# Performance work log

Hardware: AMD Instinct MI355X
Metric: run time of the kernel (lower is better)

Reference implementation:

```python
import jax, jax.numpy as jnp
import numpy as np
import math

B, N = 1, 512
C_S, C_Z = 384, 128
H, D, PQ, PV = 12, 16, 4, 8
W_C = math.sqrt(2.0 / (9.0 * PQ))
W_L = math.sqrt(1.0 / 3.0)
OUT_IN = H * D + H * PV * 3 + H * PV + H * C_Z  # 2112


def setup_inputs() -> dict:
    key = jax.random.key(0)
    ks = jax.random.split(key, 16)
    s = 0.02
    return {
        "single_representation": jax.random.normal(ks[0], (B, N, C_S), jnp.float32),
        "pair_representation": jax.random.normal(ks[1], (B, N, N, C_Z), jnp.float32),
        "rotations": jax.random.normal(ks[2], (B, N, 3, 3), jnp.float32),
        "translation": jax.random.normal(ks[3], (B, N, 3), jnp.float32),
        "w_q": jax.random.normal(ks[4], (C_S, H * D), jnp.float32) * s,
        "w_k": jax.random.normal(ks[5], (C_S, H * D), jnp.float32) * s,
        "w_v": jax.random.normal(ks[6], (C_S, H * D), jnp.float32) * s,
        "w_qf": jax.random.normal(ks[7], (C_S, 3 * H * PQ), jnp.float32) * s,
        "w_kf": jax.random.normal(ks[8], (C_S, 3 * H * PQ), jnp.float32) * s,
        "w_vf": jax.random.normal(ks[9], (C_S, 3 * H * PV), jnp.float32) * s,
        "w_bias": jax.random.normal(ks[10], (C_Z, H), jnp.float32) * s,
        "head_weights": jnp.zeros((H,), jnp.float32),
        "w_out": jax.random.normal(ks[11], (OUT_IN, C_S), jnp.float32) * s,
        "b_out": jnp.zeros((C_S,), jnp.float32),
    }


def reference(single_representation, pair_representation, rotations, translation,
              w_q, w_k, w_v, w_qf, w_kf, w_vf, w_bias, head_weights, w_out, b_out):
    s = single_representation
    z = pair_representation
    b, n, _ = s.shape

    # scalar q/k/v  [b, n, H, D]
    Q = (s @ w_q).reshape(b, n, H, D)
    K = (s @ w_k).reshape(b, n, H, D)
    V = (s @ w_v).reshape(b, n, H, D)

    # point q/k/v in local frames  [b, n, H, P, 3]
    Qf = (s @ w_qf).reshape(b, n, H, PQ, 3)
    Kf = (s @ w_kf).reshape(b, n, H, PQ, 3)
    Vf = (s @ w_vf).reshape(b, n, H, PV, 3)

    bias = z @ w_bias  # [b, n, n, H]

    # lift points to the global frame
    gq = jnp.einsum('biop,bihqp->bihqo', rotations, Qf) + translation[:, :, None, None, :]
    gk = jnp.einsum('biop,bihqp->bihqo', rotations, Kf) + translation[:, :, None, None, :]

    diff = gq[:, :, None] - gk[:, None]            # [b, i, j, H, PQ, 3]
    gamma = jax.nn.softplus(head_weights)          # [H]
    point_scores = (-0.5 * W_C) * gamma[None, None, None, :] * jnp.sum(diff * diff, axis=(-1, -2))

    rep_scores = jnp.einsum('bihd,bjhd->bijh', Q, K) / math.sqrt(D) + bias
    scores = W_L * (rep_scores + point_scores)     # [b, i, j, H]
    attn = jax.nn.softmax(scores, axis=-2)         # softmax over j

    out_pair = jnp.einsum('bijh,bijd->bihd', attn, z)          # [b, n, H, C_Z]
    out_rep = jnp.einsum('bijh,bjhd->bhid', attn, V)           # [b, H, n, D]

    gv = jnp.einsum('biop,bihqp->bihqo', rotations, Vf) + translation[:, :, None, None, :]
    tmp = jnp.einsum('bijh,bjhqo->bhiqo', attn, gv)            # [b, H, n, PV, 3]

    R_inv = jnp.swapaxes(rotations, -1, -2)
    t_inv = -jnp.einsum('bira,bia->bir', R_inv, translation)
    out_vals = jnp.einsum('biop,bhiqp->bhiqo', R_inv, tmp) + t_inv[:, None, :, None, :]

    out_rep = jnp.transpose(out_rep, (0, 2, 1, 3)).reshape(b, n, H * D)
    out_vals = jnp.transpose(out_vals, (0, 2, 1, 3, 4)).reshape(b, n, H * PV * 3)
    out_norms = jnp.sqrt(jnp.sum(out_vals.reshape(b, n, H * PV, 3) ** 2, axis=-1) + 1e-8)
    out_pair = out_pair.reshape(b, n, H * C_Z)

    cat = jnp.concatenate([out_rep, out_vals, out_norms, out_pair], axis=-1)
    return cat @ w_out + b_out
```

## Files before the change

### kernel.cpp

```cpp
#include <hip/hip_runtime.h>
#include <math.h>

#define N    512
#define CS   384
#define CZ   128
#define H    12
#define D    16
#define PQ   4
#define PV   8
#define CAT_W 2112

#define WC 0.23570226039551584f
#define WL 0.5773502691896258f

#define O_Q    0
#define O_KT   98304
#define O_VT   196608
#define O_QF   294912
#define O_KF   368640
#define O_VF   442368
#define O_GQ   589824
#define O_GKT  663552
#define O_GVT  737280
#define O_BIAS 884736
#define O_PART O_BIAS
#define O_CAT  4030464

#define KSPLIT 8
#define KCH    264
#define ALD    516

__global__ __launch_bounds__(256) void k_proj(
    const float* __restrict__ s,
    const float* __restrict__ wq, const float* __restrict__ wk,
    const float* __restrict__ wv, const float* __restrict__ wqf,
    const float* __restrict__ wkf, const float* __restrict__ wvf,
    float* __restrict__ ws) {
  int id = blockIdx.x * 256 + threadIdx.x;
  int i = id / 1152, p = id % 1152;
  const float* w; int col, W; float* dst;
  if (p < 192)      { w = wq;  col = p;     W = 192; dst = ws + O_Q  + i*192 + col; }
  else if (p < 384) { w = wk;  col = p-192; W = 192; dst = ws + O_KT + col*512 + i; }
  else if (p < 576) { w = wv;  col = p-384; W = 192; dst = ws + O_VT + col*512 + i; }
  else if (p < 720) { w = wqf; col = p-576; W = 144; dst = ws + O_QF + i*144 + col; }
  else if (p < 864) { w = wkf; col = p-720; W = 144; dst = ws + O_KF + i*144 + col; }
  else              { w = wvf; col = p-864; W = 288; dst = ws + O_VF + i*288 + col; }
  const float* srow = s + i*CS;
  float acc = 0.f;
  #pragma unroll 8
  for (int k = 0; k < CS; ++k) acc += srow[k] * w[k*W + col];
  *dst = acc;
}

__global__ __launch_bounds__(256) void k_lift(
    const float* __restrict__ rot, const float* __restrict__ trans,
    float* __restrict__ ws) {
  int id = blockIdx.x * 256 + threadIdx.x;
  int i = id / 192, pt = id % 192;
  const float* R = rot + i*9;
  const float* T = trans + i*3;
  if (pt < 48) {
    const float* src = ws + O_QF + i*144 + pt*3;
    float l0 = src[0], l1 = src[1], l2 = src[2];
    float* dst = ws + O_GQ + i*144 + pt*3;
    #pragma unroll
    for (int o = 0; o < 3; ++o)
      dst[o] = R[o*3+0]*l0 + R[o*3+1]*l1 + R[o*3+2]*l2 + T[o];
  } else if (pt < 96) {
    int p3 = pt - 48;
    const float* src = ws + O_KF + i*144 + p3*3;
    float l0 = src[0], l1 = src[1], l2 = src[2];
    #pragma unroll
    for (int o = 0; o < 3; ++o)
      ws[O_GKT + (p3*3+o)*512 + i] = R[o*3+0]*l0 + R[o*3+1]*l1 + R[o*3+2]*l2 + T[o];
  } else {
    int p3 = pt - 96;
    const float* src = ws + O_VF + i*288 + p3*3;
    float l0 = src[0], l1 = src[1], l2 = src[2];
    #pragma unroll
    for (int o = 0; o < 3; ++o)
      ws[O_GVT + (p3*3+o)*512 + i] = R[o*3+0]*l0 + R[o*3+1]*l1 + R[o*3+2]*l2 + T[o];
  }
}

__global__ __launch_bounds__(256) void k_bias(
    const float* __restrict__ z, const float* __restrict__ wb,
    float* __restrict__ ws) {
  __shared__ float wbl[CZ*H];
  int t = threadIdx.x;
  for (int idx = t; idx < CZ*H; idx += 256) wbl[idx] = wb[idx];
  __syncthreads();
  int row = blockIdx.x * 64 + (t >> 2);
  int q = t & 3;
  const float4* zr = (const float4*)(z + (size_t)row * CZ) + q;
  float acc[H];
  #pragma unroll
  for (int h = 0; h < H; ++h) acc[h] = 0.f;
  #pragma unroll
  for (int kk = 0; kk < 8; ++kk) {
    float4 v = zr[kk*4];
    int c = (q + kk*4) * 4;
    #pragma unroll
    for (int h = 0; h < H; ++h)
      acc[h] += v.x*wbl[(c+0)*H+h] + v.y*wbl[(c+1)*H+h]
              + v.z*wbl[(c+2)*H+h] + v.w*wbl[(c+3)*H+h];
  }
  #pragma unroll
  for (int h = 0; h < H; ++h) {
    acc[h] += __shfl_xor(acc[h], 1);
    acc[h] += __shfl_xor(acc[h], 2);
  }
  if (q == 0) {
    int i = row >> 9, j = row & 511;
    float* bT = ws + O_BIAS + (size_t)i*6144 + j;
    #pragma unroll
    for (int h = 0; h < H; ++h) bT[(size_t)h*512] = acc[h];
  }
}

__global__ __launch_bounds__(256) void k_score(
    const float* __restrict__ hw, float* __restrict__ ws) {
  __shared__ float Qi[192];
  __shared__ float gqi[144];
  __shared__ float coef[H];
  int i = blockIdx.x;
  int t = threadIdx.x;
  int wave = t >> 6, lane = t & 63;
  if (t < 192) Qi[t]  = ws[O_Q  + (size_t)i*192 + t];
  if (t < 144) gqi[t] = ws[O_GQ + (size_t)i*144 + t];
  if (t < H) {
    float x = hw[t];
    float sp = fmaxf(x, 0.f) + log1pf(__expf(-fabsf(x)));
    coef[t] = -0.5f * WC * sp;
  }
  __syncthreads();
  float* att = ws + O_BIAS + (size_t)i*6144;
  const float* Kt  = ws + O_KT;
  const float* gkT = ws + O_GKT;
  for (int hh = 0; hh < 3; ++hh) {
    int h = wave*3 + hh;
    float sreg[8];
    float cf = coef[h];
    #pragma unroll
    for (int jb = 0; jb < 8; ++jb) {
      int j = jb*64 + lane;
      float rep = 0.f;
      #pragma unroll
      for (int d = 0; d < 16; ++d) rep += Qi[h*16+d] * Kt[(h*16+d)*512 + j];
      float pt = 0.f;
      #pragma unroll
      for (int r = 0; r < 12; ++r) {
        float df = gqi[h*12+r] - gkT[(h*12+r)*512 + j];
        pt += df*df;
      }
      sreg[jb] = WL * (rep * 0.25f + att[(size_t)h*512 + j] + cf*pt);
    }
    float m = sreg[0];
    #pragma unroll
    for (int jb = 1; jb < 8; ++jb) m = fmaxf(m, sreg[jb]);
    #pragma unroll
    for (int off = 32; off; off >>= 1) m = fmaxf(m, __shfl_xor(m, off));
    float e = 0.f;
    #pragma unroll
    for (int jb = 0; jb < 8; ++jb) { sreg[jb] = __expf(sreg[jb] - m); e += sreg[jb]; }
    #pragma unroll
    for (int off = 32; off; off >>= 1) e += __shfl_xor(e, off);
    float inv = 1.f / e;
    #pragma unroll
    for (int jb = 0; jb < 8; ++jb) att[(size_t)h*512 + jb*64 + lane] = sreg[jb] * inv;
  }
}

__global__ __launch_bounds__(256) void k_apply(
    const float* __restrict__ z, const float* __restrict__ rot,
    const float* __restrict__ trans, float* __restrict__ ws) {
  __shared__ float aL[H*ALD];
  __shared__ float pairOdd[H*128];
  __shared__ float tmpP[H*PV*3];
  int i = blockIdx.x;
  int t = threadIdx.x;
  const float* attn = ws + O_BIAS + (size_t)i*6144;
  for (int idx = t; idx < 6144; idx += 256)
    aL[(idx >> 9)*ALD + (idx & 511)] = attn[idx];
  __syncthreads();
  float* cat = ws + O_CAT + (size_t)i*CAT_W;

  for (int task = t; task < 480; task += 256) {
    int u, h; const float* src;
    if (task < 192) { u = task;       h = u >> 4; src = ws + O_VT  + (size_t)u*512; }
    else            { u = task - 192; h = u / 24; src = ws + O_GVT + (size_t)u*512; }
    const float4* a4 = (const float4*)(aL + h*ALD);
    const float4* s4 = (const float4*)src;
    float4 acc4 = {0.f, 0.f, 0.f, 0.f};
    #pragma unroll 8
    for (int j4 = 0; j4 < 128; ++j4) {
      float4 a = a4[j4], v = s4[j4];
      acc4.x += a.x*v.x; acc4.y += a.y*v.y; acc4.z += a.z*v.z; acc4.w += a.w*v.w;
    }
    float acc = (acc4.x + acc4.y) + (acc4.z + acc4.w);
    if (task < 192) cat[u] = acc; else tmpP[u] = acc;
  }

  {
    int c = t & 127, g = t >> 7;
    float acc[H];
    #pragma unroll
    for (int h = 0; h < H; ++h) acc[h] = 0.f;
    const float* zr = z + (size_t)i*N*CZ + c;
    #pragma unroll 4
    for (int jj = 0; jj < 256; ++jj) {
      int j = jj*2 + g;
      float zv = zr[(size_t)j*CZ];
      #pragma unroll
      for (int h = 0; h < H; ++h) acc[h] += aL[h*ALD + j] * zv;
    }
    if (g) {
      #pragma unroll
      for (int h = 0; h < H; ++h) pairOdd[h*128 + c] = acc[h];
    }
    __syncthreads();
    if (!g) {
      #pragma unroll
      for (int h = 0; h < H; ++h) cat[576 + h*128 + c] = acc[h] + pairOdd[h*128 + c];
    }
  }

  if (t < 96) {
    int h = t >> 3, q = t & 7;
    const float* R = rot + i*9;
    float tp[3];
    #pragma unroll
    for (int p = 0; p < 3; ++p) tp[p] = tmpP[h*24 + q*3 + p] - trans[i*3 + p];
    float nrm = 1e-8f;
    #pragma unroll
    for (int o = 0; o < 3; ++o) {
      float v = R[o]*tp[0] + R[3+o]*tp[1] + R[6+o]*tp[2];
      cat[192 + h*24 + q*3 + o] = v;
      nrm += v*v;
    }
    cat[480 + h*8 + q] = sqrtf(nrm);
  }
}

__global__ __launch_bounds__(128) void k_out_part(
    const float* __restrict__ wo, const float* __restrict__ ws,
    float* __restrict__ part) {
  __shared__ float catT[KCH][16];
  int rt = blockIdx.x, ct = blockIdx.y, kc = blockIdx.z;
  int t = threadIdx.x;
  int i0 = rt * 16;
  int c  = ct * 128 + t;
  int k0 = kc * KCH;
  const float* cat = ws + O_CAT;
  for (int idx = t; idx < 16*KCH; idx += 128) {
    int r = idx / KCH, k = idx % KCH;
    catT[k][r] = cat[(size_t)(i0 + r) * CAT_W + k0 + k];
  }
  __syncthreads();
  float acc[16];
  #pragma unroll
  for (int r = 0; r < 16; ++r) acc[r] = 0.f;
  const float* wp = wo + (size_t)k0 * 384 + c;
  #pragma unroll 4
  for (int k = 0; k < KCH; ++k) {
    float wv = wp[(size_t)k * 384];
    const float* a = catT[k];
    #pragma unroll
    for (int r = 0; r < 16; ++r) acc[r] += a[r] * wv;
  }
  float* dst = part + (size_t)kc * (N*CS) + (size_t)i0 * 384 + c;
  #pragma unroll
  for (int r = 0; r < 16; ++r) dst[(size_t)r * 384] = acc[r];
}

__global__ __launch_bounds__(256) void k_out_red(
    const float* __restrict__ bo, const float* __restrict__ ws,
    float* __restrict__ out) {
  int id = blockIdx.x * 256 + threadIdx.x;
  int c4 = id % 96;
  float4 acc = ((const float4*)bo)[c4];
  const float* part = ws + O_PART;
  #pragma unroll
  for (int s = 0; s < KSPLIT; ++s) {
    float4 p = *(const float4*)(part + (size_t)s * (N*CS) + (size_t)id * 4);
    acc.x += p.x; acc.y += p.y; acc.z += p.z; acc.w += p.w;
  }
  ((float4*)out)[id] = acc;
}

extern "C" void kernel_launch(void* const* d_in, const int* in_sizes, int n_in,
                              void* d_out, int out_size, void* d_ws, size_t ws_size,
                              hipStream_t stream) {
  const float* s     = (const float*)d_in[0];
  const float* z     = (const float*)d_in[1];
  const float* rot   = (const float*)d_in[2];
  const float* trans = (const float*)d_in[3];
  const float* wq    = (const float*)d_in[4];
  const float* wk    = (const float*)d_in[5];
  const float* wv    = (const float*)d_in[6];
  const float* wqf   = (const float*)d_in[7];
  const float* wkf   = (const float*)d_in[8];
  const float* wvf   = (const float*)d_in[9];
  const float* wb    = (const float*)d_in[10];
  const float* hw    = (const float*)d_in[11];
  const float* wo    = (const float*)d_in[12];
  const float* bo    = (const float*)d_in[13];
  float* out = (float*)d_out;
  float* ws  = (float*)d_ws;

  hipLaunchKernelGGL(k_proj, dim3(512*1152/256), dim3(256), 0, stream,
                     s, wq, wk, wv, wqf, wkf, wvf, ws);
  hipLaunchKernelGGL(k_lift, dim3(512*192/256), dim3(256), 0, stream,
                     rot, trans, ws);
  hipLaunchKernelGGL(k_bias, dim3(512*512/64), dim3(256), 0, stream,
                     z, wb, ws);
  hipLaunchKernelGGL(k_score, dim3(512), dim3(256), 0, stream,
                     hw, ws);
  hipLaunchKernelGGL(k_apply, dim3(512), dim3(256), 0, stream,
                     z, rot, trans, ws);
  hipLaunchKernelGGL(k_out_part, dim3(32, 3, KSPLIT), dim3(128), 0, stream,
                     wo, ws, ws + O_PART);
  hipLaunchKernelGGL(k_out_red, dim3(192), dim3(256), 0, stream,
                     bo, ws, out);
}
```

Before: 497.6 us.

## Widen score/apply blocks to 768 threads and register-tile projection GEMV

The projection kernel now computes four output columns for two rows per thread using float4 weight loads, which raises reuse of the weight loads. The score kernel uses 768 threads, one wave per head, instead of looping over three heads per wave. The apply kernel uses 768 threads: 512 handle the V and point-value reductions split across 8 lanes with shuffle reductions, and 256 handle the pair-representation reduction using float4 z loads and shuffles. The shared-memory attention row padding changes from 516 to 520. Larger blocks may reduce occupancy, and the float4 pair accumulators add register pressure.

```diff
diff --git a/kernel.cpp b/kernel.cpp
--- a/kernel.cpp
+++ b/kernel.cpp
@@ -28,7 +28,7 @@
 
 #define KSPLIT 8
 #define KCH    264
-#define ALD    516
+#define ALD    520
 
 __global__ __launch_bounds__(256) void k_proj(
     const float* __restrict__ s,
@@ -37,19 +37,50 @@
     const float* __restrict__ wkf, const float* __restrict__ wvf,
     float* __restrict__ ws) {
   int id = blockIdx.x * 256 + threadIdx.x;
-  int i = id / 1152, p = id % 1152;
-  const float* w; int col, W; float* dst;
-  if (p < 192)      { w = wq;  col = p;     W = 192; dst = ws + O_Q  + i*192 + col; }
-  else if (p < 384) { w = wk;  col = p-192; W = 192; dst = ws + O_KT + col*512 + i; }
-  else if (p < 576) { w = wv;  col = p-384; W = 192; dst = ws + O_VT + col*512 + i; }
-  else if (p < 720) { w = wqf; col = p-576; W = 144; dst = ws + O_QF + i*144 + col; }
-  else if (p < 864) { w = wkf; col = p-720; W = 144; dst = ws + O_KF + i*144 + col; }
-  else              { w = wvf; col = p-864; W = 288; dst = ws + O_VF + i*288 + col; }
-  const float* srow = s + i*CS;
-  float acc = 0.f;
+  int i0 = id / 288;
+  int c4 = id % 288;
+  int col = c4 * 4;
+  const float* w; int cc, W, kind;
+  if (col < 192)      { w = wq;  cc = col;     W = 192; kind = 0; }
+  else if (col < 384) { w = wk;  cc = col-192; W = 192; kind = 1; }
+  else if (col < 576) { w = wv;  cc = col-384; W = 192; kind = 2; }
+  else if (col < 720) { w = wqf; cc = col-576; W = 144; kind = 3; }
+  else if (col < 864) { w = wkf; cc = col-720; W = 144; kind = 4; }
+  else                { w = wvf; cc = col-864; W = 288; kind = 5; }
+  const float* s0 = s + (size_t)i0 * CS;
+  const float* s1 = s0 + 256 * CS;
+  float4 a0 = {0,0,0,0}, a1 = {0,0,0,0};
   #pragma unroll 8
-  for (int k = 0; k < CS; ++k) acc += srow[k] * w[k*W + col];
-  *dst = acc;
+  for (int k = 0; k < CS; ++k) {
+    float4 wv4 = *(const float4*)(w + (size_t)k * W + cc);
+    float x0 = s0[k], x1 = s1[k];
+    a0.x += x0*wv4.x; a0.y += x0*wv4.y; a0.z += x0*wv4.z; a0.w += x0*wv4.w;
+    a1.x += x1*wv4.x; a1.y += x1*wv4.y; a1.z += x1*wv4.z; a1.w += x1*wv4.w;
+  }
+  int i1 = i0 + 256;
+  if (kind == 0) {
+    *(float4*)(ws + O_Q + (size_t)i0*192 + cc) = a0;
+    *(float4*)(ws + O_Q + (size_t)i1*192 + cc) = a1;
+  } else if (kind == 1) {
+    ws[O_KT + (size_t)(cc+0)*512 + i0] = a0.x; ws[O_KT + (size_t)(cc+1)*512 + i0] = a0.y;
+    ws[O_KT + (size_t)(cc+2)*512 + i0] = a0.z; ws[O_KT + (size_t)(cc+3)*512 + i0] = a0.w;
+    ws[O_KT + (size_t)(cc+0)*512 + i1] = a1.x; ws[O_KT + (size_t)(cc+1)*512 + i1] = a1.y;
+    ws[O_KT + (size_t)(cc+2)*512 + i1] = a1.z; ws[O_KT + (size_t)(cc+3)*512 + i1] = a1.w;
+  } else if (kind == 2) {
+    ws[O_VT + (size_t)(cc+0)*512 + i0] = a0.x; ws[O_VT + (size_t)(cc+1)*512 + i0] = a0.y;
+    ws[O_VT + (size_t)(cc+2)*512 + i0] = a0.z; ws[O_VT + (size_t)(cc+3)*512 + i0] = a0.w;
+    ws[O_VT + (size_t)(cc+0)*512 + i1] = a1.x; ws[O_VT + (size_t)(cc+1)*512 + i1] = a1.y;
+    ws[O_VT + (size_t)(cc+2)*512 + i1] = a1.z; ws[O_VT + (size_t)(cc+3)*512 + i1] = a1.w;
+  } else if (kind == 3) {
+    *(float4*)(ws + O_QF + (size_t)i0*144 + cc) = a0;
+    *(float4*)(ws + O_QF + (size_t)i1*144 + cc) = a1;
+  } else if (kind == 4) {
+    *(float4*)(ws + O_KF + (size_t)i0*144 + cc) = a0;
+    *(float4*)(ws + O_KF + (size_t)i1*144 + cc) = a1;
+  } else {
+    *(float4*)(ws + O_VF + (size_t)i0*288 + cc) = a0;
+    *(float4*)(ws + O_VF + (size_t)i1*288 + cc) = a1;
+  }
 }
 
 __global__ __launch_bounds__(256) void k_lift(
@@ -72,14 +103,14 @@
     float l0 = src[0], l1 = src[1], l2 = src[2];
     #pragma unroll
     for (int o = 0; o < 3; ++o)
-      ws[O_GKT + (p3*3+o)*512 + i] = R[o*3+0]*l0 + R[o*3+1]*l1 + R[o*3+2]*l2 + T[o];
+      ws[O_GKT + (size_t)(p3*3+o)*512 + i] = R[o*3+0]*l0 + R[o*3+1]*l1 + R[o*3+2]*l2 + T[o];
   } else {
     int p3 = pt - 96;
     const float* src = ws + O_VF + i*288 + p3*3;
     float l0 = src[0], l1 = src[1], l2 = src[2];
     #pragma unroll
     for (int o = 0; o < 3; ++o)
-      ws[O_GVT + (p3*3+o)*512 + i] = R[o*3+0]*l0 + R[o*3+1]*l1 + R[o*3+2]*l2 + T[o];
+      ws[O_GVT + (size_t)(p3*3+o)*512 + i] = R[o*3+0]*l0 + R[o*3+1]*l1 + R[o*3+2]*l2 + T[o];
   }
 }
 
@@ -118,112 +149,126 @@
   }
 }
 
-__global__ __launch_bounds__(256) void k_score(
+__global__ __launch_bounds__(768) void k_score(
     const float* __restrict__ hw, float* __restrict__ ws) {
   __shared__ float Qi[192];
   __shared__ float gqi[144];
-  __shared__ float coef[H];
   int i = blockIdx.x;
   int t = threadIdx.x;
-  int wave = t >> 6, lane = t & 63;
+  int h = t >> 6, lane = t & 63;
   if (t < 192) Qi[t]  = ws[O_Q  + (size_t)i*192 + t];
-  if (t < 144) gqi[t] = ws[O_GQ + (size_t)i*144 + t];
-  if (t < H) {
-    float x = hw[t];
-    float sp = fmaxf(x, 0.f) + log1pf(__expf(-fabsf(x)));
-    coef[t] = -0.5f * WC * sp;
-  }
-  __syncthreads();
-  float* att = ws + O_BIAS + (size_t)i*6144;
-  const float* Kt  = ws + O_KT;
-  const float* gkT = ws + O_GKT;
-  for (int hh = 0; hh < 3; ++hh) {
-    int h = wave*3 + hh;
-    float sreg[8];
-    float cf = coef[h];
-    #pragma unroll
-    for (int jb = 0; jb < 8; ++jb) {
-      int j = jb*64 + lane;
-      float rep = 0.f;
-      #pragma unroll
-      for (int d = 0; d < 16; ++d) rep += Qi[h*16+d] * Kt[(h*16+d)*512 + j];
-      float pt = 0.f;
-      #pragma unroll
-      for (int r = 0; r < 12; ++r) {
-        float df = gqi[h*12+r] - gkT[(h*12+r)*512 + j];
-        pt += df*df;
-      }
-      sreg[jb] = WL * (rep * 0.25f + att[(size_t)h*512 + j] + cf*pt);
-    }
-    float m = sreg[0];
-    #pragma unroll
-    for (int jb = 1; jb < 8; ++jb) m = fmaxf(m, sreg[jb]);
-    #pragma unroll
-    for (int off = 32; off; off >>= 1) m = fmaxf(m, __shfl_xor(m, off));
-    float e = 0.f;
-    #pragma unroll
-    for (int jb = 0; jb < 8; ++jb) { sreg[jb] = __expf(sreg[jb] - m); e += sreg[jb]; }
-    #pragma unroll
-    for (int off = 32; off; off >>= 1) e += __shfl_xor(e, off);
-    float inv = 1.f / e;
-    #pragma unroll
-    for (int jb = 0; jb < 8; ++jb) att[(size_t)h*512 + jb*64 + lane] = sreg[jb] * inv;
-  }
-}
-
-__global__ __launch_bounds__(256) void k_apply(
+  else if (t >= 256 && t < 400) gqi[t-256] = ws[O_GQ + (size_t)i*144 + (t-256)];
+  float x = hw[h];
+  float sp = fmaxf(x, 0.f) + log1pf(__expf(-fabsf(x)));
+  float cf = -0.5f * WC * sp;
+  __syncthreads();
+  float* att = ws + O_BIAS + (size_t)i*6144 + (size_t)h*512;
+  const float* Kt  = ws + O_KT  + (size_t)h*16*512;
+  const float* gkT = ws + O_GKT + (size_t)h*12*512;
+  const float* Qr  = Qi + h*16;
+  const float* gqr = gqi + h*12;
+  float sreg[8];
+  #pragma unroll
+  for (int jb = 0; jb < 8; ++jb) {
+    int j = jb*64 + lane;
+    float rep = 0.f;
+    #pragma unroll
+    for (int d = 0; d < 16; ++d) rep += Qr[d] * Kt[(size_t)d*512 + j];
+    float pt = 0.f;
+    #pragma unroll
+    for (int r = 0; r < 12; ++r) {
+      float df = gqr[r] - gkT[(size_t)r*512 + j];
+      pt += df*df;
+    }
+    sreg[jb] = WL * (rep * 0.25f + att[j] + cf*pt);
+  }
+  float m = sreg[0];
+  #pragma unroll
+  for (int jb = 1; jb < 8; ++jb) m = fmaxf(m, sreg[jb]);
+  #pragma unroll
+  for (int off = 32; off; off >>= 1) m = fmaxf(m, __shfl_xor(m, off));
+  float e = 0.f;
+  #pragma unroll
+  for (int jb = 0; jb < 8; ++jb) { sreg[jb] = __expf(sreg[jb] - m); e += sreg[jb]; }
+  #pragma unroll
+  for (int off = 32; off; off >>= 1) e += __shfl_xor(e, off);
+  float inv = 1.f / e;
+  #pragma unroll
+  for (int jb = 0; jb < 8; ++jb) att[jb*64 + lane] = sreg[jb] * inv;
+}
+
+__global__ __launch_bounds__(768) void k_apply2(
     const float* __restrict__ z, const float* __restrict__ rot,
     const float* __restrict__ trans, float* __restrict__ ws) {
   __shared__ float aL[H*ALD];
-  __shared__ float pairOdd[H*128];
   __shared__ float tmpP[H*PV*3];
   int i = blockIdx.x;
   int t = threadIdx.x;
   const float* attn = ws + O_BIAS + (size_t)i*6144;
-  for (int idx = t; idx < 6144; idx += 256)
+  for (int idx = t; idx < 6144; idx += 768)
     aL[(idx >> 9)*ALD + (idx & 511)] = attn[idx];
   __syncthreads();
   float* cat = ws + O_CAT + (size_t)i*CAT_W;
 
-  for (int task = t; task < 480; task += 256) {
-    int u, h; const float* src;
-    if (task < 192) { u = task;       h = u >> 4; src = ws + O_VT  + (size_t)u*512; }
-    else            { u = task - 192; h = u / 24; src = ws + O_GVT + (size_t)u*512; }
-    const float4* a4 = (const float4*)(aL + h*ALD);
-    const float4* s4 = (const float4*)src;
-    float4 acc4 = {0.f, 0.f, 0.f, 0.f};
-    #pragma unroll 8
-    for (int j4 = 0; j4 < 128; ++j4) {
-      float4 a = a4[j4], v = s4[j4];
-      acc4.x += a.x*v.x; acc4.y += a.y*v.y; acc4.z += a.z*v.z; acc4.w += a.w*v.w;
-    }
-    float acc = (acc4.x + acc4.y) + (acc4.z + acc4.w);
-    if (task < 192) cat[u] = acc; else tmpP[u] = acc;
-  }
-
-  {
-    int c = t & 127, g = t >> 7;
-    float acc[H];
-    #pragma unroll
-    for (int h = 0; h < H; ++h) acc[h] = 0.f;
-    const float* zr = z + (size_t)i*N*CZ + c;
+  if (t < 512) {
+    int u0 = t >> 3, jg = t & 7;
+    for (int round = 0; round < 8; ++round) {
+      int u = round*64 + u0;
+      if (u < 480) {
+        int h; const float* src;
+        if (u < 192) { h = u >> 4;            src = ws + O_VT  + (size_t)u*512; }
+        else         { int v = u-192; h = v/24; src = ws + O_GVT + (size_t)v*512; }
+        const float4* s4 = (const float4*)src;
+        const float4* a4 = (const float4*)(aL + h*ALD);
+        float4 acc = {0,0,0,0};
+        #pragma unroll
+        for (int jj = 0; jj < 16; ++jj) {
+          int j4 = jj*8 + jg;
+          float4 a = a4[j4], v = s4[j4];
+          acc.x += a.x*v.x; acc.y += a.y*v.y; acc.z += a.z*v.z; acc.w += a.w*v.w;
+        }
+        float r = (acc.x + acc.y) + (acc.z + acc.w);
+        r += __shfl_xor(r, 1); r += __shfl_xor(r, 2); r += __shfl_xor(r, 4);
+        if (jg == 0) {
+          if (u < 192) cat[u] = r; else tmpP[u-192] = r;
+        }
+      }
+    }
+  } else {
+    int tp = t - 512;
+    int jg = tp & 7, c4 = tp >> 3;
+    const float4* z4 = (const float4*)(z + (size_t)i*N*CZ);
+    float4 pacc[H];
+    #pragma unroll
+    for (int h = 0; h < H; ++h) pacc[h] = make_float4(0.f,0.f,0.f,0.f);
     #pragma unroll 4
-    for (int jj = 0; jj < 256; ++jj) {
-      int j = jj*2 + g;
-      float zv = zr[(size_t)j*CZ];
+    for (int jj = 0; jj < 64; ++jj) {
+      int j = jj*8 + jg;
+      float4 zv = z4[j*32 + c4];
       #pragma unroll
-      for (int h = 0; h < H; ++h) acc[h] += aL[h*ALD + j] * zv;
-    }
-    if (g) {
+      for (int h = 0; h < H; ++h) {
+        float a = aL[h*ALD + j];
+        pacc[h].x += a*zv.x; pacc[h].y += a*zv.y;
+        pacc[h].z += a*zv.z; pacc[h].w += a*zv.w;
+      }
+    }
+    #pragma unroll
+    for (int h = 0; h < H; ++h) {
       #pragma unroll
-      for (int h = 0; h < H; ++h) pairOdd[h*128 + c] = acc[h];
-    }
-    __syncthreads();
-    if (!g) {
+      for (int off = 1; off <= 4; off <<= 1) {
+        pacc[h].x += __shfl_xor(pacc[h].x, off);
+        pacc[h].y += __shfl_xor(pacc[h].y, off);
+        pacc[h].z += __shfl_xor(pacc[h].z, off);
+        pacc[h].w += __shfl_xor(pacc[h].w, off);
+      }
+    }
+    if (jg == 0) {
+      float4* dst = (float4*)(cat + 576);
       #pragma unroll
-      for (int h = 0; h < H; ++h) cat[576 + h*128 + c] = acc[h] + pairOdd[h*128 + c];
-    }
-  }
+      for (int h = 0; h < H; ++h) dst[h*32 + c4] = pacc[h];
+    }
+  }
+  __syncthreads();
 
   if (t < 96) {
     int h = t >> 3, q = t & 7;
@@ -308,15 +353,15 @@
   float* out = (float*)d_out;
   float* ws  = (float*)d_ws;
 
-  hipLaunchKernelGGL(k_proj, dim3(512*1152/256), dim3(256), 0, stream,
+  hipLaunchKernelGGL(k_proj, dim3(288), dim3(256), 0, stream,
                      s, wq, wk, wv, wqf, wkf, wvf, ws);
-  hipLaunchKernelGGL(k_lift, dim3(512*192/256), dim3(256), 0, stream,
+  hipLaunchKernelGGL(k_lift, dim3(384), dim3(256), 0, stream,
                      rot, trans, ws);
-  hipLaunchKernelGGL(k_bias, dim3(512*512/64), dim3(256), 0, stream,
+  hipLaunchKernelGGL(k_bias, dim3(4096), dim3(256), 0, stream,
                      z, wb, ws);
-  hipLaunchKernelGGL(k_score, dim3(512), dim3(256), 0, stream,
+  hipLaunchKernelGGL(k_score, dim3(512), dim3(768), 0, stream,
                      hw, ws);
-  hipLaunchKernelGGL(k_apply, dim3(512), dim3(256), 0, stream,
+  hipLaunchKernelGGL(k_apply2, dim3(512), dim3(768), 0, stream,
                      z, rot, trans, ws);
   hipLaunchKernelGGL(k_out_part, dim3(32, 3, KSPLIT), dim3(128), 0, stream,
                      wo, ws, ws + O_PART);
```

Measured after the change: 398.2 us. 1.25x faster.
